# Optimization experiments

Hardware: AMD Instinct MI355X
Metric: run time of the kernel (lower is better)

Reference implementation:

```python
import jax, jax.numpy as jnp
import numpy as np

G, D, H = 64, 16, 8   # n groups, per-group input dim, GRU hidden (feat_dim)
B, T = 64, 512


def setup_inputs() -> dict:
    key = jax.random.key(0)
    ks = jax.random.split(key, 5)
    s = 1.0 / np.sqrt(H)  # PyTorch GRU init: U(-1/sqrt(hidden), 1/sqrt(hidden))
    x = jax.random.normal(ks[0], (B, T, G * D), dtype=jnp.float32)
    W_ih = jax.random.uniform(ks[1], (G, 3 * H, D), jnp.float32, -s, s)
    W_hh = jax.random.uniform(ks[2], (G, 3 * H, H), jnp.float32, -s, s)
    b_ih = jax.random.uniform(ks[3], (G, 3 * H), jnp.float32, -s, s)
    b_hh = jax.random.uniform(ks[4], (G, 3 * H), jnp.float32, -s, s)
    return {"x": x, "W_ih": W_ih, "W_hh": W_hh, "b_ih": b_ih, "b_hh": b_hh}


def reference(x, W_ih, W_hh, b_ih, b_hh):
    # x: [B, T, G*D] -> per-group GRU, output [B, T, G, H]
    Bq, Tq, _ = x.shape
    xg = x.reshape(Bq, Tq, G, D)
    # Precompute all input-to-hidden gate projections as one grouped GEMM.
    gx = jnp.einsum('btgd,gkd->btgk', xg, W_ih) + b_ih  # [B, T, G, 3H]
    gx = jnp.moveaxis(gx, 1, 0)                          # [T, B, G, 3H]
    h0 = jnp.zeros((Bq, G, H), dtype=x.dtype)

    def step(h, gxt):
        gh = jnp.einsum('bgh,gkh->bgk', h, W_hh) + b_hh  # [B, G, 3H]
        xr, xz, xn = jnp.split(gxt, 3, axis=-1)          # PyTorch gate order: r, z, n
        hr, hz, hn = jnp.split(gh, 3, axis=-1)
        r = jax.nn.sigmoid(xr + hr)
        z = jax.nn.sigmoid(xz + hz)
        n = jnp.tanh(xn + r * hn)
        h_new = (1.0 - z) * n + z * h
        return h_new, h_new

    _, hs = jax.lax.scan(step, h0, gx)  # hs: [T, B, G, H]
    return jnp.moveaxis(hs, 0, 1)       # [B, T, G, H]
```

## Files before the change

### kernel.cpp

```cpp
#include <hip/hip_runtime.h>


#define Gn 64
#define Dn 16
#define Hn 8
#define Tn 512
#define CHUNK 8
#define NCH (Tn / CHUNK)

typedef float v2f __attribute__((ext_vector_type(2)));

__device__ __forceinline__ float rcp_fast(float v) { return __builtin_amdgcn_rcpf(v); }
__device__ __forceinline__ float exp2_fast(float v) { return __builtin_amdgcn_exp2f(v); }

#define KNL (-1.44269504088896340736f)
#define KP2 ( 2.88539008177792681472f)

template <int CTRL>
__device__ __forceinline__ float dppf(float v) {
    return __int_as_float(
        __builtin_amdgcn_update_dpp(0, __float_as_int(v), CTRL, 0xF, 0xF, false));
}
template <int CTRL>
__device__ __forceinline__ v2f dpp2(v2f v) {
    v2f r;
    r.x = dppf<CTRL>(v.x);
    r.y = dppf<CTRL>(v.y);
    return r;
}

__device__ __forceinline__ void sync_lds() {
    asm volatile("s_waitcnt lgkmcnt(0)" ::: "memory");
    __builtin_amdgcn_s_barrier();
}

__global__ __attribute__((amdgpu_flat_work_group_size(128, 128),
                          amdgpu_waves_per_eu(1, 1)))
void mcgru_kernel(
    const float* __restrict__ x,
    const float* __restrict__ W_ih,
    const float* __restrict__ W_hh,
    const float* __restrict__ b_ih,
    const float* __restrict__ b_hh,
    float* __restrict__ out)
{
    __shared__ float gxs[2][CHUNK][3][64];

    const int tlane = threadIdx.x & 63;
    const int wid   = threadIdx.x >> 6;
    const int c     = tlane >> 3;
    const int u     = tlane & 7;
    const int cell  = blockIdx.x * 8 + c;
    const int g     = cell & (Gn - 1);
    const int b     = cell >> 6;
    const int s4 = u & 3, q = u >> 2;

    int jmap[8];
#pragma unroll
    for (int k = 0; k < 8; ++k) {
        const int hi2 = k >> 2, r = k & 3;
        jmap[k] = ((q ^ hi2) << 2) | (s4 ^ r ^ (hi2 ? 3 : 0));
    }
    const float scale[3] = {KNL, KNL, KP2};

    if (wid == 1) {
        v2f wih[3][8];
        float bs[3];
#pragma unroll
        for (int qg = 0; qg < 3; ++qg) {
            const int row = qg * Hn + u;
            const float sc = scale[qg];
            const float* wr = W_ih + ((size_t)g * 24 + row) * Dn;
#pragma unroll
            for (int k = 0; k < 8; ++k) {
                const int dp = jmap[k] * 2;
                wih[qg][k] = (v2f){wr[dp] * sc, wr[dp + 1] * sc};
            }
            bs[qg] = (qg < 2)
                ? (b_ih[g * 24 + row] + b_hh[g * 24 + row]) * sc
                : b_ih[g * 24 + row] * sc;
        }
#pragma unroll
        for (int qg = 0; qg < 3; ++qg) {
#pragma unroll
            for (int i = 0; i < 8; ++i) asm volatile("" : "+v"(wih[qg][i]));
            asm volatile("" : "+v"(bs[qg]));
        }

        const float* xq = x + ((size_t)b * Tn * Gn + g) * Dn + 2 * u;
        auto load_x = [&](int t) -> v2f {
            return *(const v2f*)(xq + (size_t)t * (Gn * Dn));
        };
        auto proj_store = [&](v2f xv, float* dst) {
            v2f X[8];
            X[0] = xv;
            X[1] = dpp2<0xB1>(xv);
            X[2] = dpp2<0x4E>(xv);
            X[3] = dpp2<0x1B>(xv);
            X[4] = dpp2<0x141>(X[0]);
            X[5] = dpp2<0x141>(X[1]);
            X[6] = dpp2<0x141>(X[2]);
            X[7] = dpp2<0x141>(X[3]);
#pragma unroll
            for (int qg = 0; qg < 3; ++qg) {
                v2f acc = wih[qg][0] * X[0];
#pragma unroll
                for (int i = 1; i < 8; ++i) acc += wih[qg][i] * X[i];
                dst[qg * 64] = (bs[qg] + acc.x) + acc.y;
            }
        };

        v2f xrA[CHUNK], xrB[CHUNK];
#pragma unroll
        for (int j = 0; j < CHUNK; ++j) xrA[j] = load_x(j);
#pragma unroll
        for (int j = 0; j < CHUNK; ++j) xrB[j] = load_x(CHUNK + j);
#pragma unroll
        for (int j = 0; j < CHUNK; ++j)
            proj_store(xrA[j], &gxs[0][j][0][tlane]);
        sync_lds();

        for (int k = 0; k < NCH; k += 2) {
            if (k + 1 < NCH) {
#pragma unroll
                for (int j = 0; j < CHUNK; ++j)
                    proj_store(xrB[j], &gxs[1][j][0][tlane]);
            }
            if (k + 2 < NCH) {
#pragma unroll
                for (int j = 0; j < CHUNK; ++j)
                    xrA[j] = load_x((k + 2) * CHUNK + j);
            }
            sync_lds();
            if (k + 2 < NCH) {
#pragma unroll
                for (int j = 0; j < CHUNK; ++j)
                    proj_store(xrA[j], &gxs[0][j][0][tlane]);
            }
            if (k + 3 < NCH) {
#pragma unroll
                for (int j = 0; j < CHUNK; ++j)
                    xrB[j] = load_x((k + 3) * CHUNK + j);
            }
            sync_lds();
        }
    } else {
        float whh[3][8], bhn;
#pragma unroll
        for (int qg = 0; qg < 3; ++qg) {
            const int row = qg * Hn + u;
            const float sc = scale[qg];
            const float* hrow = W_hh + ((size_t)g * 24 + row) * Hn;
#pragma unroll
            for (int k = 0; k < 8; ++k) whh[qg][k] = hrow[jmap[k]] * sc;
        }
        bhn = b_hh[g * 24 + 2 * Hn + u] * KP2;
#pragma unroll
        for (int qg = 0; qg < 3; ++qg)
#pragma unroll
            for (int k = 0; k < 8; ++k) asm volatile("" : "+v"(whh[qg][k]));
        asm volatile("" : "+v"(bhn));

        float* op = out + ((size_t)b * Tn * Gn + g) * Hn + u;
        float h = 0.0f;
        sync_lds();

        for (int k = 0; k < NCH; ++k) {
            const float* bufp = &gxs[k & 1][0][0][tlane];
#pragma unroll
            for (int j = 0; j < CHUNK; ++j) {
                const float gx0 = bufp[(j * 3 + 0) * 64];
                const float gx1 = bufp[(j * 3 + 1) * 64];
                const float gx2 = bufp[(j * 3 + 2) * 64];

                float H[8];
                H[0] = h;
                H[1] = dppf<0xB1>(h);
                H[2] = dppf<0x4E>(h);
                H[3] = dppf<0x1B>(h);
                H[4] = dppf<0x141>(H[0]);
                H[5] = dppf<0x141>(H[1]);
                H[6] = dppf<0x141>(H[2]);
                H[7] = dppf<0x141>(H[3]);

                float gh[3];
#pragma unroll
                for (int qg = 0; qg < 3; ++qg) {
                    float a = fmaf(whh[qg][1], H[1], whh[qg][0] * H[0]);
                    a = fmaf(whh[qg][2], H[2], a);
                    a = fmaf(whh[qg][3], H[3], a);
                    float cc = (qg == 2) ? fmaf(whh[qg][4], H[4], bhn)
                                         : whh[qg][4] * H[4];
                    cc = fmaf(whh[qg][5], H[5], cc);
                    cc = fmaf(whh[qg][6], H[6], cc);
                    cc = fmaf(whh[qg][7], H[7], cc);
                    gh[qg] = a + cc;
                }
                const float r  = rcp_fast(1.0f + exp2_fast(gx0 + gh[0]));
                const float z  = rcp_fast(1.0f + exp2_fast(gx1 + gh[1]));
                const float zh = z * h;
                const float om = 1.0f - z;
                const float e  = exp2_fast(fmaf(r, gh[2], gx2));
                const float n  = fmaf(-2.0f, rcp_fast(e + 1.0f), 1.0f);
                h = fmaf(n, om, zh);
                __builtin_nontemporal_store(
                    h, op + (size_t)(k * CHUNK + j) * (Gn * Hn));
            }
            sync_lds();
        }
    }
}

extern "C" void kernel_launch(void* const* d_in, const int* in_sizes, int n_in,
                              void* d_out, int out_size, void* d_ws, size_t ws_size,
                              hipStream_t stream) {
    const float* x    = (const float*)d_in[0];
    const float* W_ih = (const float*)d_in[1];
    const float* W_hh = (const float*)d_in[2];
    const float* b_ih = (const float*)d_in[3];
    const float* b_hh = (const float*)d_in[4];
    float* out = (float*)d_out;

    dim3 grid(512), block(128);
    hipLaunchKernelGGL(mcgru_kernel, grid, block, 0, stream,
                       x, W_ih, W_hh, b_ih, b_hh, out);
}
```

Measured before the change: 268.4 us.

## Interleave two independent GRU cells per recurrence wave to hide latency

Each block now handles 16 cells using three waves: two producer waves compute input projections, and one recurrence wave advances two independent cell groups (A and B) together. This gives the serial recurrence chain instruction-level parallelism, so the exp/rcp/DPP latency of one chain can overlap with the other. The grid is halved to 256 blocks, and LDS gate values for the next step are prefetched one step ahead. In exchange, the recurrence wave uses more registers and only half as many blocks are launched, which may leave compute units idle on a large GPU.

```diff
diff --git a/kernel.cpp b/kernel.cpp
--- a/kernel.cpp
+++ b/kernel.cpp
@@ -34,7 +34,7 @@
     __builtin_amdgcn_s_barrier();
 }
 
-__global__ __attribute__((amdgpu_flat_work_group_size(128, 128),
+__global__ __attribute__((amdgpu_flat_work_group_size(192, 192),
                           amdgpu_waves_per_eu(1, 1)))
 void mcgru_kernel(
     const float* __restrict__ x,
@@ -44,15 +44,12 @@
     const float* __restrict__ b_hh,
     float* __restrict__ out)
 {
-    __shared__ float gxs[2][CHUNK][3][64];
+    __shared__ float gxs[2][CHUNK][3][128];
 
     const int tlane = threadIdx.x & 63;
     const int wid   = threadIdx.x >> 6;
     const int c     = tlane >> 3;
     const int u     = tlane & 7;
-    const int cell  = blockIdx.x * 8 + c;
-    const int g     = cell & (Gn - 1);
-    const int b     = cell >> 6;
     const int s4 = u & 3, q = u >> 2;
 
     int jmap[8];
@@ -63,7 +60,11 @@
     }
     const float scale[3] = {KNL, KNL, KP2};
 
-    if (wid == 1) {
+    if (wid >= 1) {
+        const int cell = blockIdx.x * 16 + (wid - 1) * 8 + c;
+        const int g    = cell & (Gn - 1);
+        const int b    = cell >> 6;
+
         v2f wih[3][8];
         float bs[3];
 #pragma unroll
@@ -87,6 +88,7 @@
             asm volatile("" : "+v"(bs[qg]));
         }
 
+        const int lds_off = (wid - 1) * 64 + tlane;
         const float* xq = x + ((size_t)b * Tn * Gn + g) * Dn + 2 * u;
         auto load_x = [&](int t) -> v2f {
             return *(const v2f*)(xq + (size_t)t * (Gn * Dn));
@@ -106,7 +108,7 @@
                 v2f acc = wih[qg][0] * X[0];
 #pragma unroll
                 for (int i = 1; i < 8; ++i) acc += wih[qg][i] * X[i];
-                dst[qg * 64] = (bs[qg] + acc.x) + acc.y;
+                dst[qg * 128] = (bs[qg] + acc.x) + acc.y;
             }
         };
 
@@ -117,14 +119,14 @@
         for (int j = 0; j < CHUNK; ++j) xrB[j] = load_x(CHUNK + j);
 #pragma unroll
         for (int j = 0; j < CHUNK; ++j)
-            proj_store(xrA[j], &gxs[0][j][0][tlane]);
+            proj_store(xrA[j], &gxs[0][j][0][lds_off]);
         sync_lds();
 
         for (int k = 0; k < NCH; k += 2) {
             if (k + 1 < NCH) {
 #pragma unroll
                 for (int j = 0; j < CHUNK; ++j)
-                    proj_store(xrB[j], &gxs[1][j][0][tlane]);
+                    proj_store(xrB[j], &gxs[1][j][0][lds_off]);
             }
             if (k + 2 < NCH) {
 #pragma unroll
@@ -135,7 +137,7 @@
             if (k + 2 < NCH) {
 #pragma unroll
                 for (int j = 0; j < CHUNK; ++j)
-                    proj_store(xrA[j], &gxs[0][j][0][tlane]);
+                    proj_store(xrA[j], &gxs[0][j][0][lds_off]);
             }
             if (k + 3 < NCH) {
 #pragma unroll
@@ -145,66 +147,116 @@
             sync_lds();
         }
     } else {
-        float whh[3][8], bhn;
+        const int cellA = blockIdx.x * 16 + c;
+        const int cellB = cellA + 8;
+        const int gA = cellA & (Gn - 1), bA = cellA >> 6;
+        const int gB = cellB & (Gn - 1), bB = cellB >> 6;
+
+        float whhA[3][8], whhB[3][8], bhnA, bhnB;
 #pragma unroll
         for (int qg = 0; qg < 3; ++qg) {
             const int row = qg * Hn + u;
             const float sc = scale[qg];
-            const float* hrow = W_hh + ((size_t)g * 24 + row) * Hn;
-#pragma unroll
-            for (int k = 0; k < 8; ++k) whh[qg][k] = hrow[jmap[k]] * sc;
-        }
-        bhn = b_hh[g * 24 + 2 * Hn + u] * KP2;
+            const float* hrA = W_hh + ((size_t)gA * 24 + row) * Hn;
+            const float* hrB = W_hh + ((size_t)gB * 24 + row) * Hn;
+#pragma unroll
+            for (int k = 0; k < 8; ++k) {
+                whhA[qg][k] = hrA[jmap[k]] * sc;
+                whhB[qg][k] = hrB[jmap[k]] * sc;
+            }
+        }
+        bhnA = b_hh[gA * 24 + 2 * Hn + u] * KP2;
+        bhnB = b_hh[gB * 24 + 2 * Hn + u] * KP2;
 #pragma unroll
         for (int qg = 0; qg < 3; ++qg)
 #pragma unroll
-            for (int k = 0; k < 8; ++k) asm volatile("" : "+v"(whh[qg][k]));
-        asm volatile("" : "+v"(bhn));
-
-        float* op = out + ((size_t)b * Tn * Gn + g) * Hn + u;
-        float h = 0.0f;
+            for (int k = 0; k < 8; ++k) {
+                asm volatile("" : "+v"(whhA[qg][k]));
+                asm volatile("" : "+v"(whhB[qg][k]));
+            }
+        asm volatile("" : "+v"(bhnA));
+        asm volatile("" : "+v"(bhnB));
+
+        float* opA = out + ((size_t)bA * Tn * Gn + gA) * Hn + u;
+        float* opB = out + ((size_t)bB * Tn * Gn + gB) * Hn + u;
+        float hA = 0.0f, hB = 0.0f;
         sync_lds();
 
         for (int k = 0; k < NCH; ++k) {
-            const float* bufp = &gxs[k & 1][0][0][tlane];
+            const float* bufp = &gxs[k & 1][0][0][0];
+            float aA[3], aB[3], nA[3], nB[3];
+#pragma unroll
+            for (int qg = 0; qg < 3; ++qg) {
+                aA[qg] = bufp[qg * 128 + tlane];
+                aB[qg] = bufp[qg * 128 + 64 + tlane];
+            }
 #pragma unroll
             for (int j = 0; j < CHUNK; ++j) {
-                const float gx0 = bufp[(j * 3 + 0) * 64];
-                const float gx1 = bufp[(j * 3 + 1) * 64];
-                const float gx2 = bufp[(j * 3 + 2) * 64];
-
-                float H[8];
-                H[0] = h;
-                H[1] = dppf<0xB1>(h);
-                H[2] = dppf<0x4E>(h);
-                H[3] = dppf<0x1B>(h);
-                H[4] = dppf<0x141>(H[0]);
-                H[5] = dppf<0x141>(H[1]);
-                H[6] = dppf<0x141>(H[2]);
-                H[7] = dppf<0x141>(H[3]);
-
-                float gh[3];
+                if (j + 1 < CHUNK) {
+#pragma unroll
+                    for (int qg = 0; qg < 3; ++qg) {
+                        nA[qg] = bufp[((j + 1) * 3 + qg) * 128 + tlane];
+                        nB[qg] = bufp[((j + 1) * 3 + qg) * 128 + 64 + tlane];
+                    }
+                }
+                float HA[8], HB[8];
+                HA[0] = hA;               HB[0] = hB;
+                HA[1] = dppf<0xB1>(hA);   HB[1] = dppf<0xB1>(hB);
+                HA[2] = dppf<0x4E>(hA);   HB[2] = dppf<0x4E>(hB);
+                HA[3] = dppf<0x1B>(hA);   HB[3] = dppf<0x1B>(hB);
+                HA[4] = dppf<0x141>(HA[0]); HB[4] = dppf<0x141>(HB[0]);
+                HA[5] = dppf<0x141>(HA[1]); HB[5] = dppf<0x141>(HB[1]);
+                HA[6] = dppf<0x141>(HA[2]); HB[6] = dppf<0x141>(HB[2]);
+                HA[7] = dppf<0x141>(HA[3]); HB[7] = dppf<0x141>(HB[3]);
+
+                float ghA[3], ghB[3];
 #pragma unroll
                 for (int qg = 0; qg < 3; ++qg) {
-                    float a = fmaf(whh[qg][1], H[1], whh[qg][0] * H[0]);
-                    a = fmaf(whh[qg][2], H[2], a);
-                    a = fmaf(whh[qg][3], H[3], a);
-                    float cc = (qg == 2) ? fmaf(whh[qg][4], H[4], bhn)
-                                         : whh[qg][4] * H[4];
-                    cc = fmaf(whh[qg][5], H[5], cc);
-                    cc = fmaf(whh[qg][6], H[6], cc);
-                    cc = fmaf(whh[qg][7], H[7], cc);
-                    gh[qg] = a + cc;
+                    float a1 = fmaf(whhA[qg][1], HA[1], whhA[qg][0] * HA[0]);
+                    float b1 = fmaf(whhB[qg][1], HB[1], whhB[qg][0] * HB[0]);
+                    a1 = fmaf(whhA[qg][2], HA[2], a1);
+                    b1 = fmaf(whhB[qg][2], HB[2], b1);
+                    a1 = fmaf(whhA[qg][3], HA[3], a1);
+                    b1 = fmaf(whhB[qg][3], HB[3], b1);
+                    float a2 = (qg == 2) ? fmaf(whhA[qg][4], HA[4], bhnA)
+                                         : whhA[qg][4] * HA[4];
+                    float b2 = (qg == 2) ? fmaf(whhB[qg][4], HB[4], bhnB)
+                                         : whhB[qg][4] * HB[4];
+                    a2 = fmaf(whhA[qg][5], HA[5], a2);
+                    b2 = fmaf(whhB[qg][5], HB[5], b2);
+                    a2 = fmaf(whhA[qg][6], HA[6], a2);
+                    b2 = fmaf(whhB[qg][6], HB[6], b2);
+                    a2 = fmaf(whhA[qg][7], HA[7], a2);
+                    b2 = fmaf(whhB[qg][7], HB[7], b2);
+                    ghA[qg] = a1 + a2;
+                    ghB[qg] = b1 + b2;
                 }
-                const float r  = rcp_fast(1.0f + exp2_fast(gx0 + gh[0]));
-                const float z  = rcp_fast(1.0f + exp2_fast(gx1 + gh[1]));
-                const float zh = z * h;
-                const float om = 1.0f - z;
-                const float e  = exp2_fast(fmaf(r, gh[2], gx2));
-                const float n  = fmaf(-2.0f, rcp_fast(e + 1.0f), 1.0f);
-                h = fmaf(n, om, zh);
-                __builtin_nontemporal_store(
-                    h, op + (size_t)(k * CHUNK + j) * (Gn * Hn));
+                const float eArA = exp2_fast(aA[0] + ghA[0]);
+                const float eBrB = exp2_fast(aB[0] + ghB[0]);
+                const float eAz  = exp2_fast(aA[1] + ghA[1]);
+                const float eBz  = exp2_fast(aB[1] + ghB[1]);
+                const float rA = rcp_fast(1.0f + eArA);
+                const float rB = rcp_fast(1.0f + eBrB);
+                const float zA = rcp_fast(1.0f + eAz);
+                const float zB = rcp_fast(1.0f + eBz);
+                const float zhA = zA * hA,    zhB = zB * hB;
+                const float omA = 1.0f - zA,  omB = 1.0f - zB;
+                const float eA = exp2_fast(fmaf(rA, ghA[2], aA[2]));
+                const float eB = exp2_fast(fmaf(rB, ghB[2], aB[2]));
+                const float nAv = fmaf(-2.0f, rcp_fast(eA + 1.0f), 1.0f);
+                const float nBv = fmaf(-2.0f, rcp_fast(eB + 1.0f), 1.0f);
+                hA = fmaf(nAv, omA, zhA);
+                hB = fmaf(nBv, omB, zhB);
+                const size_t trow = (size_t)(k * CHUNK + j) * (Gn * Hn);
+                __builtin_nontemporal_store(hA, opA + trow);
+                __builtin_nontemporal_store(hB, opB + trow);
+                if (j + 1 < CHUNK) {
+#pragma unroll
+                    for (int qg = 0; qg < 3; ++qg) {
+                        aA[qg] = nA[qg];
+                        aB[qg] = nB[qg];
+                    }
+                }
             }
             sync_lds();
         }
@@ -221,7 +273,7 @@
     const float* b_hh = (const float*)d_in[4];
     float* out = (float*)d_out;
 
-    dim3 grid(512), block(128);
+    dim3 grid(256), block(192);
     hipLaunchKernelGGL(mcgru_kernel, grid, block, 0, stream,
                        x, W_ih, W_hh, b_ih, b_hh, out);
 }
```

Result: no change. 272.5 us (+1.5%).
